# Kernel tuning notes

Hardware: AMD Instinct MI355X
Metric: run time of the kernel (lower is better)

## Reference

```python
import jax, jax.numpy as jnp
import numpy as np

BAND = 8          # band_width
DS = 0.1          # diag_subtract
DILATIONS = (1, 2, 4)
EPS_NORM = 1e-6
EPS_GAP = 1e-6
EPS_LN = 1e-5


def _conv1d(x, w, b, dil=1):
    # x: (B, C_in, T), w: (C_out, C_in, K) torch-style OIH
    pad = dil * (w.shape[-1] // 2)  # 'same' padding as in torch module
    y = jax.lax.conv_general_dilated(
        x, w, window_strides=(1,), padding=[(pad, pad)],
        rhs_dilation=(dil,), dimension_numbers=("NCH", "OIH", "NCH"))
    return y + b[None, :, None]


def _strip(feat, mask, w, ds):
    # Banded cosine SSM: strip[b, idx, t] = ((xn[b,t].xn[b,t+|k|]) - ds*[k==0] + 1)/2 * m[t]*m[t+|k|]
    # Mathematically identical to full S = xn xn^T (symmetric) followed by
    # extract_diagonal_strip, but computes only the (2w+1)-wide band.
    xm = feat * mask[:, :, None]
    xn = xm / (jnp.linalg.norm(xm, axis=-1, keepdims=True) + EPS_NORM)
    T = xn.shape[1]
    rows = []
    for k in range(-w, w + 1):
        a = abs(k)
        dot = jnp.einsum("btd,btd->bt", xn[:, :T - a] if a else xn, xn[:, a:])
        s = (dot - (ds if k == 0 else 0.0) + 1.0) * 0.5
        s = s * mask[:, :T - a] * mask[:, a:] if a else s * mask * mask
        rows.append(jnp.pad(s, ((0, 0), (0, a))))
    return jnp.stack(rows, axis=1)  # (B, 2w+1, T)


def _encode(strip, mask, w_in, b_in, stages):
    h = jax.nn.relu(_conv1d(strip, w_in, b_in))
    for (wd, bd, wp, bp, d) in stages:
        h = jax.nn.relu(_conv1d(h, wd, bd, d))   # dilated k=3 conv (dropout=eval no-op)
        h = jax.nn.relu(_conv1d(h, wp, bp))      # pointwise k=1 conv
    m = mask[:, None, :]
    return (h * m).sum(-1) / (m.sum(-1) + EPS_GAP)  # masked GAP -> (B, C)


def setup_inputs() -> dict:
    key = jax.random.key(0)
    ks = jax.random.split(key, 32)
    B, T, D, C, NB = 32, 4096, 256, 64, 2 * BAND + 1
    s = 0.02
    n = lambda k, shp: (jax.random.normal(k, shp, jnp.float32) * s)
    inp = {
        "video_feat": jax.random.normal(ks[0], (B, T, D), jnp.float32),
        "audio_feat": jax.random.normal(ks[1], (B, T, D), jnp.float32),
        "video_mask": jnp.ones((B, T), jnp.float32),
        "audio_mask": jnp.ones((B, T), jnp.float32),
        "w_in": n(ks[2], (C, NB, 1)), "b_in": jnp.zeros((C,), jnp.float32),
        "w_d1": n(ks[3], (C, C, 3)), "b_d1": jnp.zeros((C,), jnp.float32),
        "w_p1": n(ks[4], (C, C, 1)), "b_p1": jnp.zeros((C,), jnp.float32),
        "w_d2": n(ks[5], (C, C, 3)), "b_d2": jnp.zeros((C,), jnp.float32),
        "w_p2": n(ks[6], (C, C, 1)), "b_p2": jnp.zeros((C,), jnp.float32),
        "w_d3": n(ks[7], (C, C, 3)), "b_d3": jnp.zeros((C,), jnp.float32),
        "w_p3": n(ks[8], (C, C, 1)), "b_p3": jnp.zeros((C,), jnp.float32),
        "ln_g": jnp.ones((2 * C,), jnp.float32), "ln_b": jnp.zeros((2 * C,), jnp.float32),
        "mha_w1": n(ks[9], (2 * C, C)), "mha_b1": jnp.zeros((C,), jnp.float32),
        "mha_w2": n(ks[10], (C, 1)), "mha_b2": -jnp.ones((1,), jnp.float32),
        "ffn_w1": n(ks[11], (2 * C, C)), "ffn_b1": jnp.zeros((C,), jnp.float32),
        "ffn_w2": n(ks[12], (C, 1)), "ffn_b2": jnp.zeros((1,), jnp.float32),
    }
    return inp


def reference(video_feat, audio_feat, video_mask, audio_mask,
              w_in, b_in, w_d1, b_d1, w_p1, b_p1, w_d2, b_d2, w_p2, b_p2,
              w_d3, b_d3, w_p3, b_p3, ln_g, ln_b,
              mha_w1, mha_b1, mha_w2, mha_b2, ffn_w1, ffn_b1, ffn_w2, ffn_b2):
    stages = [(w_d1, b_d1, w_p1, b_p1, DILATIONS[0]),
              (w_d2, b_d2, w_p2, b_p2, DILATIONS[1]),
              (w_d3, b_d3, w_p3, b_p3, DILATIONS[2])]
    z_a = _encode(_strip(audio_feat, audio_mask, BAND, DS), audio_mask, w_in, b_in, stages)
    z_v = _encode(_strip(video_feat, video_mask, BAND, DS), video_mask, w_in, b_in, stages)
    f = jnp.concatenate([z_a, z_v], axis=-1)  # (B, 2C), audio first as in torch
    mu = f.mean(-1, keepdims=True)
    var = ((f - mu) ** 2).mean(-1, keepdims=True)
    fn = (f - mu) / jnp.sqrt(var + EPS_LN) * ln_g + ln_b
    g_mha = jax.nn.sigmoid(jax.nn.relu(fn @ mha_w1 + mha_b1) @ mha_w2 + mha_b2)
    g_ffn = jnp.tanh(jax.nn.relu(fn @ ffn_w1 + ffn_b1) @ ffn_w2 + ffn_b2)
    return (g_mha[:, :, None], g_ffn[:, :, None])  # (B,1,1) each
```

## Files before the change

kernel.cpp:

```cpp
#include <hip/hip_runtime.h>
#include <math.h>

#define B_ 32
#define T_ 4096
#define D_ 256
#define C_ 64
#define EPSN 1e-6f
#define EPSG 1e-6f
#define EPSL 1e-5f
#define DS_ 0.1f

typedef short bfrag __attribute__((ext_vector_type(8)));
typedef float f32x4 __attribute__((ext_vector_type(4)));
typedef unsigned short ushort4_t __attribute__((ext_vector_type(4)));
typedef unsigned short ushort8_t __attribute__((ext_vector_type(8)));

static __device__ __forceinline__ unsigned short f2bf(float f) {
    unsigned int u = __builtin_bit_cast(unsigned int, f);
    unsigned int r = u + 0x7fffu + ((u >> 16) & 1u);
    return (unsigned short)(r >> 16);
}
static __device__ __forceinline__ float bf2f(unsigned short u) {
    return __builtin_bit_cast(float, ((unsigned int)u) << 16);
}

static __device__ __forceinline__ f32x4 mfma_bf16(bfrag a, bfrag b, f32x4 c) {
    return __builtin_amdgcn_mfma_f32_16x16x32_bf16(a, b, c, 0, 0, 0);
}

static __device__ __forceinline__ bfrag cvt8(float4 lo, float4 hi) {
    bfrag v;
    v[0] = (short)f2bf(lo.x); v[1] = (short)f2bf(lo.y);
    v[2] = (short)f2bf(lo.z); v[3] = (short)f2bf(lo.w);
    v[4] = (short)f2bf(hi.x); v[5] = (short)f2bf(hi.y);
    v[6] = (short)f2bf(hi.z); v[7] = (short)f2bf(hi.w);
    return v;
}

static __device__ __forceinline__ unsigned int cvtpk(float a, float b) {
    unsigned int r;
    asm("v_cvt_pk_bf16_f32 %0, %1, %2" : "=v"(r) : "v"(a), "v"(b));
    return r;
}

#define GLD16(dst, base, OFF) \
    asm volatile("global_load_dwordx4 %0, %1, off offset:" #OFF \
                 : "=v"(dst) : "v"(base))

__global__ __launch_bounds__(256) void prepack_kernel(
    const float* __restrict__ w_in,
    const float* __restrict__ wd0, const float* __restrict__ wp0,
    const float* __restrict__ wd1, const float* __restrict__ wp1,
    const float* __restrict__ wd2, const float* __restrict__ wp2,
    unsigned short* __restrict__ wk)
{
    int idx = blockIdx.x * 256 + threadIdx.x;
    if (idx >= 1024 + 3 * 16384) return;
    if (idx < 1024) {
        int c = idx >> 4, a = idx & 15;
        float wv = 0.f;
        if (a <= 8) {
            wv = w_in[c * 17 + 8 + a];
            if (a > 0) wv += w_in[c * 17 + 8 - a];
        }
        wk[idx] = f2bf(wv);
    } else {
        int i2 = idx - 1024;
        int s = i2 >> 14;
        int r = i2 & 16383;
        const float* wd = s == 0 ? wd0 : (s == 1 ? wd1 : wd2);
        const float* wp = s == 0 ? wp0 : (s == 1 ? wp1 : wp2);
        unsigned short v;
        if (r < 12288) {
            int c = r / 192, k = r - c * 192;
            int tap = k >> 6, ci = k & 63;
            v = f2bf(wd[c * 192 + ci * 3 + tap]);
        } else {
            v = f2bf(wp[r - 12288]);
        }
        wk[idx] = v;
    }
}

#define SEQB 22
#define TPB 2

__global__ __launch_bounds__(256, 2) void strip_kernel(
    const float* __restrict__ feat0, const float* __restrict__ mask0,
    const float* __restrict__ feat1, const float* __restrict__ mask1,
    unsigned short* __restrict__ s16g)
{
    __shared__ float dotbuf[4 * 864];
    __shared__ float sclw[4 * 32];
    __shared__ float mskb[208];

    int bid0 = blockIdx.x;
    int bid  = (bid0 & 7) * 176 + (bid0 >> 3);
    int seq  = bid / SEQB;
    int blk  = bid - seq * SEQB;
    int b    = seq & 31;
    int mod  = seq >> 5;
    int mb   = mod * B_ + b;
    const float* feat = mod ? feat1 : feat0;
    const float* mask = mod ? mask1 : mask0;
    int first = blk * TPB;
    int ngr   = (43 - first < TPB) ? (43 - first) : TPB;
    int base0 = first * 96;
    int tid = threadIdx.x;
    int w = tid >> 6, lane = tid & 63;
    int l15 = lane & 15, lg = lane >> 4;

    if (tid < 208) {
        int tg = base0 + tid;
        mskb[tid] = (tg < T_) ? mask[(size_t)b * T_ + tg] : 0.f;
    }
    __syncthreads();

    const float* fb = feat + (size_t)b * T_ * D_;

    float4 fa0[8], fb0[8], fa1[8], fb1[8];
    const float *pA, *pB;

    auto setaddr = [&](int g) {
        int i0 = (first + g) * 96 + 24 * w;
        int tA = i0 + l15;      if (tA >= T_) tA = 0;
        int tB = i0 + 16 + l15; if (tB >= T_) tB = 0;
        pA = fb + (size_t)tA * D_ + lg * 8;
        pB = fb + (size_t)tB * D_ + lg * 8;
    };

#define ISSUE_C0() do { \
    GLD16(fa0[0], pA, 0);   GLD16(fb0[0], pB, 0);   \
    GLD16(fa0[1], pA, 16);  GLD16(fb0[1], pB, 16);  \
    GLD16(fa0[2], pA, 128); GLD16(fb0[2], pB, 128); \
    GLD16(fa0[3], pA, 144); GLD16(fb0[3], pB, 144); \
    GLD16(fa0[4], pA, 256); GLD16(fb0[4], pB, 256); \
    GLD16(fa0[5], pA, 272); GLD16(fb0[5], pB, 272); \
    GLD16(fa0[6], pA, 384); GLD16(fb0[6], pB, 384); \
    GLD16(fa0[7], pA, 400); GLD16(fb0[7], pB, 400); } while (0)

#define ISSUE_C1() do { \
    GLD16(fa1[0], pA, 512); GLD16(fb1[0], pB, 512); \
    GLD16(fa1[1], pA, 528); GLD16(fb1[1], pB, 528); \
    GLD16(fa1[2], pA, 640); GLD16(fb1[2], pB, 640); \
    GLD16(fa1[3], pA, 656); GLD16(fb1[3], pB, 656); \
    GLD16(fa1[4], pA, 768); GLD16(fb1[4], pB, 768); \
    GLD16(fa1[5], pA, 784); GLD16(fb1[5], pB, 784); \
    GLD16(fa1[6], pA, 896); GLD16(fb1[6], pB, 896); \
    GLD16(fa1[7], pA, 912); GLD16(fb1[7], pB, 912); } while (0)

    setaddr(0);
    ISSUE_C0();
    ISSUE_C1();

    for (int g = 0; g < ngr; ++g) {
        bool nxt = (g + 1 < ngr);

        __builtin_amdgcn_sched_barrier(0);
        asm volatile("s_waitcnt vmcnt(16)" ::: "memory");
        __builtin_amdgcn_sched_barrier(0);

        f32x4 a00 = {0.f, 0.f, 0.f, 0.f};
        f32x4 a01 = {0.f, 0.f, 0.f, 0.f};
        f32x4 a11 = {0.f, 0.f, 0.f, 0.f};
        #pragma unroll
        for (int ks = 0; ks < 4; ++ks) {
            bfrag av = cvt8(fa0[2 * ks], fa0[2 * ks + 1]);
            bfrag bv = cvt8(fb0[2 * ks], fb0[2 * ks + 1]);
            a00 = mfma_bf16(av, av, a00);
            a01 = mfma_bf16(av, bv, a01);
            a11 = mfma_bf16(bv, bv, a11);
        }

        if (nxt) { setaddr(g + 1); ISSUE_C0(); }

        __builtin_amdgcn_sched_barrier(0);
        if (nxt) asm volatile("s_waitcnt vmcnt(16)" ::: "memory");
        else     asm volatile("s_waitcnt vmcnt(0)"  ::: "memory");
        __builtin_amdgcn_sched_barrier(0);

        #pragma unroll
        for (int ks = 0; ks < 4; ++ks) {
            bfrag av = cvt8(fa1[2 * ks], fa1[2 * ks + 1]);
            bfrag bv = cvt8(fb1[2 * ks], fb1[2 * ks + 1]);
            a00 = mfma_bf16(av, av, a00);
            a01 = mfma_bf16(av, bv, a01);
            a11 = mfma_bf16(bv, bv, a11);
        }

        if (nxt) ISSUE_C1();

        int i0 = (first + g) * 96 + 24 * w;
        float* bb = dotbuf + w * 864;
        #pragma unroll
        for (int r = 0; r < 4; ++r) {
            int row = lg * 4 + r;
            bb[row * 18 + l15] = a00[r];
            bb[288 + row * 18 + l15] = a01[r];
            bb[576 + row * 18 + l15] = a11[r];
        }
        if (lane < 32) {
            int v = lane;
            float sd = (v < 16) ? bb[v * 18 + v] : bb[576 + (v - 16) * 18 + (v - 16)];
            float m = mskb[i0 - base0 + v];
            sclw[w * 32 + v] = m / (m * sqrtf(sd) + EPSN);
        }
        if (lane < 24) {
            int r = lane;
            int tglob = i0 + r;
            if (tglob < T_) {
                int rel = i0 - base0 + r;
                float m_t = mskb[rel], sc_t = sclw[w * 32 + r];
                ushort8_t o0, o1;
                #pragma unroll
                for (int e = 0; e < 8; ++e) { o0[e] = 0; o1[e] = 0; }
                #pragma unroll
                for (int a = 0; a <= 8; ++a) {
                    int c = r + a;
                    float dot;
                    if (r < 8)       dot = bb[r * 18 + c];
                    else if (r < 16) dot = (c < 16) ? bb[r * 18 + c]
                                                   : bb[288 + r * 18 + (c - 16)];
                    else             dot = bb[576 + (r - 16) * 18 + (c - 16)];
                    float dn = dot * sc_t * sclw[w * 32 + r + a];
                    float s = (dn - (a == 0 ? DS_ : 0.f) + 1.f) * 0.5f * m_t * mskb[rel + a];
                    if (a < 8) o0[a] = f2bf(s); else o1[0] = f2bf(s);
                }
                unsigned short* dst = s16g + ((size_t)mb * T_ + tglob) * 16;
                *(ushort8_t*)dst = o0;
                *(ushort8_t*)(dst + 8) = o1;
            }
        }
    }
#undef ISSUE_C0
#undef ISSUE_C1
}

#define TT 128
#define G_ 16
#define WB 160
#define OFF_BUFA 1024
#define OFF_BUFB 21504
#define SMEM_TOT (41984 + 512)

static __device__ __forceinline__ int swzi(int row, int su, int off) {
    return row * 64 + ((su ^ (row & 7)) << 3) + off;
}

static __device__ __forceinline__ void emit4(unsigned short* dst, f32x4 acc, bool valid) {
    float v0 = valid ? fmaxf(acc[0], 0.f) : 0.f;
    float v1 = valid ? fmaxf(acc[1], 0.f) : 0.f;
    float v2 = valid ? fmaxf(acc[2], 0.f) : 0.f;
    float v3 = valid ? fmaxf(acc[3], 0.f) : 0.f;
    uint2 p;
    p.x = cvtpk(v0, v1);
    p.y = cvtpk(v2, v3);
    *(uint2*)dst = p;
}

template<int DIL>
static __device__ __forceinline__ void conv_stage(
    const unsigned short* __restrict__ wdg, const unsigned short* __restrict__ wpg,
    unsigned short* __restrict__ bufIn, unsigned short* __restrict__ bufOut,
    const float* __restrict__ b_d, const float* __restrict__ b_p,
    int t0, int l15, int lg, int mt0, int wn)
{
    {
        bfrag ad[2][6];
        f32x4 bd[2];
        #pragma unroll
        for (int m = 0; m < 2; ++m) {
            int row = (mt0 + m) * 16 + l15;
            #pragma unroll
            for (int ks = 0; ks < 6; ++ks) {
                int tap = ks >> 1, half = ks & 1;
                ad[m][ks] = *(const bfrag*)(wdg + row * 192 + tap * 64 + half * 32 + lg * 8);
            }
            #pragma unroll
            for (int r = 0; r < 4; ++r) bd[m][r] = b_d[(mt0 + m) * 16 + lg * 4 + r];
        }
        for (int nt = wn * 5; nt < wn * 5 + 5; ++nt) {
            int j = nt * 16 + l15;
            f32x4 acc0 = bd[0], acc1 = bd[1];
            #pragma unroll
            for (int ks = 0; ks < 6; ++ks) {
                int tap = ks >> 1, half = ks & 1;
                int brow = j + (tap - 1) * DIL;
                bfrag bv = *(const bfrag*)(bufIn + swzi(brow, half * 4 + lg, 0));
                acc0 = mfma_bf16(ad[0][ks], bv, acc0);
                acc1 = mfma_bf16(ad[1][ks], bv, acc1);
            }
            int tg = t0 - G_ + j;
            bool valid = (tg >= 0 && tg < T_);
            emit4(bufOut + swzi(j, (mt0 + 0) * 2 + (lg >> 1), (lg & 1) * 4), acc0, valid);
            emit4(bufOut + swzi(j, (mt0 + 1) * 2 + (lg >> 1), (lg & 1) * 4), acc1, valid);
        }
    }
    __syncthreads();

    {
        bfrag ap[2][2];
        f32x4 bp[2];
        #pragma unroll
        for (int m = 0; m < 2; ++m) {
            int row = (mt0 + m) * 16 + l15;
            #pragma unroll
            for (int half = 0; half < 2; ++half)
                ap[m][half] = *(const bfrag*)(wpg + row * 64 + half * 32 + lg * 8);
            #pragma unroll
            for (int r = 0; r < 4; ++r) bp[m][r] = b_p[(mt0 + m) * 16 + lg * 4 + r];
        }
        for (int nt = wn * 5; nt < wn * 5 + 5; ++nt) {
            int j = nt * 16 + l15;
            f32x4 acc0 = bp[0], acc1 = bp[1];
            #pragma unroll
            for (int half = 0; half < 2; ++half) {
                bfrag bv = *(const bfrag*)(bufOut + swzi(j, half * 4 + lg, 0));
                acc0 = mfma_bf16(ap[0][half], bv, acc0);
                acc1 = mfma_bf16(ap[1][half], bv, acc1);
            }
            int tg = t0 - G_ + j;
            bool valid = (tg >= 0 && tg < T_);
            emit4(bufIn + swzi(j, (mt0 + 0) * 2 + (lg >> 1), (lg & 1) * 4), acc0, valid);
            emit4(bufIn + swzi(j, (mt0 + 1) * 2 + (lg >> 1), (lg & 1) * 4), acc1, valid);
        }
    }
    __syncthreads();
}

__global__ __launch_bounds__(256, 3) void conv_mfma_kernel(
    const unsigned short* __restrict__ s16g,
    const float* __restrict__ mask0, const float* __restrict__ mask1,
    const unsigned short* __restrict__ wk,
    const float* __restrict__ b_in,
    const float* __restrict__ b_d1, const float* __restrict__ b_p1,
    const float* __restrict__ b_d2, const float* __restrict__ b_p2,
    const float* __restrict__ b_d3, const float* __restrict__ b_p3,
    float* __restrict__ z_part)
{
    __shared__ __align__(16) char smem[SMEM_TOT];
    float* red = (float*)smem;
    unsigned short* bufA = (unsigned short*)(smem + OFF_BUFA);
    unsigned short* bufB = (unsigned short*)(smem + OFF_BUFB);

    int bid  = blockIdx.x;
    int tile = bid & 31;
    int b    = (bid >> 5) & 31;
    int mod  = bid >> 10;
    int mb   = mod * B_ + b;
    const float* mask = mod ? mask1 : mask0;
    int t0  = tile * TT;
    int tid = threadIdx.x;
    int lane = tid & 63;
    int w = tid >> 6;
    int l15 = lane & 15, lg = lane >> 4;
    int wm = w >> 1, wn = w & 1;
    int mt0 = wm * 2;

    {
        const unsigned short* srow = s16g + (size_t)mb * T_ * 16;
        int lg2 = lg & 1;
        bfrag a_in[2];
        f32x4 bi[2];
        #pragma unroll
        for (int m = 0; m < 2; ++m) {
            int row = (mt0 + m) * 16 + l15;
            a_in[m] = *(const bfrag*)(wk + row * 16 + lg2 * 8);
            #pragma unroll
            for (int r = 0; r < 4; ++r) bi[m][r] = b_in[(mt0 + m) * 16 + lg * 4 + r];
        }
        for (int nt = wn * 5; nt < wn * 5 + 5; ++nt) {
            int j = nt * 16 + l15;
            int tg = t0 - G_ + j;
            bool valid = (tg >= 0 && tg < T_);
            bfrag bv = {0, 0, 0, 0, 0, 0, 0, 0};
            if (lg < 2 && valid) bv = *(const bfrag*)(srow + (size_t)tg * 16 + lg * 8);
            f32x4 acc0 = bi[0], acc1 = bi[1];
            acc0 = mfma_bf16(a_in[0], bv, acc0);
            acc1 = mfma_bf16(a_in[1], bv, acc1);
            emit4(bufA + swzi(j, (mt0 + 0) * 2 + (lg >> 1), (lg & 1) * 4), acc0, valid);
            emit4(bufA + swzi(j, (mt0 + 1) * 2 + (lg >> 1), (lg & 1) * 4), acc1, valid);
        }
    }
    __syncthreads();

    conv_stage<1>(wk + 1024,             wk + 1024 + 12288,             bufA, bufB, b_d1, b_p1, t0, l15, lg, mt0, wn);
    conv_stage<2>(wk + 1024 + 16384,     wk + 1024 + 16384 + 12288,     bufA, bufB, b_d2, b_p2, t0, l15, lg, mt0, wn);
    conv_stage<4>(wk + 1024 + 2 * 16384, wk + 1024 + 2 * 16384 + 12288, bufA, bufB, b_d3, b_p3, t0, l15, lg, mt0, wn);

    {
        int c = tid & 63, g = tid >> 6;
        const float* mrow = mask + (size_t)b * T_ + t0;
        float acc = 0.f;
        #pragma unroll 4
        for (int i = 0; i < 32; ++i) {
            int jj = g * 32 + i;
            int r = G_ + jj;
            acc += bf2f(bufA[swzi(r, c >> 3, c & 7)]) * mrow[jj];
        }
        red[g * 64 + c] = acc;
    }
    __syncthreads();
    if (tid < 64) {
        float z = red[tid] + red[64 + tid] + red[128 + tid] + red[192 + tid];
        z_part[((size_t)mb * 32 + tile) * 64 + tid] = z;
    }
}

__global__ __launch_bounds__(128) void gates_kernel(
    const float* __restrict__ z_part,
    const float* __restrict__ mask0, const float* __restrict__ mask1,
    const float* __restrict__ ln_g, const float* __restrict__ ln_b,
    const float* __restrict__ mha_w1, const float* __restrict__ mha_b1,
    const float* __restrict__ mha_w2, const float* __restrict__ mha_b2,
    const float* __restrict__ ffn_w1, const float* __restrict__ ffn_b1,
    const float* __restrict__ ffn_w2, const float* __restrict__ ffn_b2,
    float* __restrict__ out)
{
    __shared__ float fn[128];
    __shared__ float red[4];
    __shared__ float msum[2];
    int b = blockIdx.x, tid = threadIdx.x;
    int mod = tid >> 6, c = tid & 63;

    float z = 0.f;
    for (int tl = 0; tl < 32; ++tl)
        z += z_part[((size_t)(mod * B_ + b) * 32 + tl) * 64 + c];

    const float* mk = mod ? mask1 : mask0;
    float ms = 0.f;
    for (int t = c; t < T_; t += 64) ms += mk[(size_t)b * T_ + t];
    #pragma unroll
    for (int o = 32; o > 0; o >>= 1) ms += __shfl_xor(ms, o);
    if (c == 0) msum[mod] = ms;
    __syncthreads();

    float fv = z / (msum[mod] + EPSG);
    float s1 = fv, s2 = fv * fv;
    #pragma unroll
    for (int o = 32; o > 0; o >>= 1) { s1 += __shfl_xor(s1, o); s2 += __shfl_xor(s2, o); }
    if (c == 0) { red[mod * 2] = s1; red[mod * 2 + 1] = s2; }
    __syncthreads();

    float mu  = (red[0] + red[2]) * (1.0f / 128.0f);
    float ex2 = (red[1] + red[3]) * (1.0f / 128.0f);
    float var = ex2 - mu * mu;
    float fnv = (fv - mu) * rsqrtf(var + EPSL) * ln_g[tid] + ln_b[tid];
    fn[tid] = fnv;
    __syncthreads();

    const float* W1 = mod ? ffn_w1 : mha_w1;
    const float* B1 = mod ? ffn_b1 : mha_b1;
    const float* W2 = mod ? ffn_w2 : mha_w2;
    const float* B2 = mod ? ffn_b2 : mha_b2;
    float r = B1[c];
    for (int i = 0; i < 128; ++i) r += fn[i] * W1[i * 64 + c];
    r = fmaxf(r, 0.f);
    float g = r * W2[c];
    #pragma unroll
    for (int o = 32; o > 0; o >>= 1) g += __shfl_xor(g, o);
    if (c == 0) {
        g += B2[0];
        out[mod * B_ + b] = mod ? tanhf(g) : 1.0f / (1.0f + expf(-g));
    }
}

extern "C" void kernel_launch(void* const* d_in, const int* in_sizes, int n_in,
                              void* d_out, int out_size, void* d_ws, size_t ws_size,
                              hipStream_t stream) {
    const float* video_feat = (const float*)d_in[0];
    const float* audio_feat = (const float*)d_in[1];
    const float* video_mask = (const float*)d_in[2];
    const float* audio_mask = (const float*)d_in[3];
    const float* w_in = (const float*)d_in[4];
    const float* b_in = (const float*)d_in[5];
    const float* w_d1 = (const float*)d_in[6];
    const float* b_d1 = (const float*)d_in[7];
    const float* w_p1 = (const float*)d_in[8];
    const float* b_p1 = (const float*)d_in[9];
    const float* w_d2 = (const float*)d_in[10];
    const float* b_d2 = (const float*)d_in[11];
    const float* w_p2 = (const float*)d_in[12];
    const float* b_p2 = (const float*)d_in[13];
    const float* w_d3 = (const float*)d_in[14];
    const float* b_d3 = (const float*)d_in[15];
    const float* w_p3 = (const float*)d_in[16];
    const float* b_p3 = (const float*)d_in[17];
    const float* ln_g = (const float*)d_in[18];
    const float* ln_b = (const float*)d_in[19];
    const float* mha_w1 = (const float*)d_in[20];
    const float* mha_b1 = (const float*)d_in[21];
    const float* mha_w2 = (const float*)d_in[22];
    const float* mha_b2 = (const float*)d_in[23];
    const float* ffn_w1 = (const float*)d_in[24];
    const float* ffn_b1 = (const float*)d_in[25];
    const float* ffn_w2 = (const float*)d_in[26];
    const float* ffn_b2 = (const float*)d_in[27];

    unsigned short* s16g = (unsigned short*)d_ws;
    float* z_part = (float*)((char*)d_ws + (size_t)2 * B_ * T_ * 16 * 2);
    unsigned short* wk = (unsigned short*)((char*)z_part + (size_t)2 * B_ * 32 * 64 * 4);

    prepack_kernel<<<dim3(196), dim3(256), 0, stream>>>(
        w_in, w_d1, w_p1, w_d2, w_p2, w_d3, w_p3, wk);

    strip_kernel<<<dim3(64 * SEQB), dim3(256), 0, stream>>>(
        audio_feat, audio_mask, video_feat, video_mask, s16g);

    conv_mfma_kernel<<<dim3(2 * B_ * (T_ / TT)), dim3(256), 0, stream>>>(
        s16g, audio_mask, video_mask, wk, b_in,
        b_d1, b_p1, b_d2, b_p2, b_d3, b_p3, z_part);

    gates_kernel<<<dim3(B_), dim3(128), 0, stream>>>(
        z_part, audio_mask, video_mask, ln_g, ln_b,
        mha_w1, mha_b1, mha_w2, mha_b2, ffn_w1, ffn_b1, ffn_w2, ffn_b2,
        (float*)d_out);
}
```

Baseline: 144.7 us.

## Fuse banded cosine strip computation into conv encoder kernel via LDS

Merges the strip kernel into the conv encoder kernel so each 128-step tile computes its own strip rows (with a 16-step halo) directly into shared memory instead of writing a bf16 strip tensor to global memory and reading it back. This removes one kernel launch and the global round trip of the strip intermediate. In exchange, halo rows are recomputed per tile (176 rows for 128 outputs), so feature reads and MFMA dot work grow, and shared memory use per block rises.

After: 189.0 us. 1.31x slower.

```diff
diff --git a/kernel.cpp b/kernel.cpp
--- a/kernel.cpp
+++ b/kernel.cpp
@@ -82,52 +82,155 @@
     }
 }
 
-#define SEQB 22
-#define TPB 2
-
-__global__ __launch_bounds__(256, 2) void strip_kernel(
+#define TT 128
+#define G_ 16
+#define OFF_BUFA 1024
+#define OFF_BUFB 21504
+#define OFF_SBUF 41984
+#define OFF_MSKB 47360
+#define SMEM_TOT 48576
+
+static __device__ __forceinline__ int swzi(int row, int su, int off) {
+    return row * 64 + ((su ^ (row & 7)) << 3) + off;
+}
+
+static __device__ __forceinline__ void emit4(unsigned short* dst, f32x4 acc, bool valid) {
+    float v0 = valid ? fmaxf(acc[0], 0.f) : 0.f;
+    float v1 = valid ? fmaxf(acc[1], 0.f) : 0.f;
+    float v2 = valid ? fmaxf(acc[2], 0.f) : 0.f;
+    float v3 = valid ? fmaxf(acc[3], 0.f) : 0.f;
+    uint2 p;
+    p.x = cvtpk(v0, v1);
+    p.y = cvtpk(v2, v3);
+    *(uint2*)dst = p;
+}
+
+template<int DIL>
+static __device__ __forceinline__ void conv_stage(
+    const unsigned short* __restrict__ wdg, const unsigned short* __restrict__ wpg,
+    unsigned short* __restrict__ bufIn, unsigned short* __restrict__ bufOut,
+    const float* __restrict__ b_d, const float* __restrict__ b_p,
+    int t0, int l15, int lg, int mt0, int wn)
+{
+    {
+        bfrag ad[2][6];
+        f32x4 bd[2];
+        #pragma unroll
+        for (int m = 0; m < 2; ++m) {
+            int row = (mt0 + m) * 16 + l15;
+            #pragma unroll
+            for (int ks = 0; ks < 6; ++ks) {
+                int tap = ks >> 1, half = ks & 1;
+                ad[m][ks] = *(const bfrag*)(wdg + row * 192 + tap * 64 + half * 32 + lg * 8);
+            }
+            #pragma unroll
+            for (int r = 0; r < 4; ++r) bd[m][r] = b_d[(mt0 + m) * 16 + lg * 4 + r];
+        }
+        for (int nt = wn * 5; nt < wn * 5 + 5; ++nt) {
+            int j = nt * 16 + l15;
+            f32x4 acc0 = bd[0], acc1 = bd[1];
+            #pragma unroll
+            for (int ks = 0; ks < 6; ++ks) {
+                int tap = ks >> 1, half = ks & 1;
+                int brow = j + (tap - 1) * DIL;
+                bfrag bv = *(const bfrag*)(bufIn + swzi(brow, half * 4 + lg, 0));
+                acc0 = mfma_bf16(ad[0][ks], bv, acc0);
+                acc1 = mfma_bf16(ad[1][ks], bv, acc1);
+            }
+            int tg = t0 - G_ + j;
+            bool valid = (tg >= 0 && tg < T_);
+            emit4(bufOut + swzi(j, (mt0 + 0) * 2 + (lg >> 1), (lg & 1) * 4), acc0, valid);
+            emit4(bufOut + swzi(j, (mt0 + 1) * 2 + (lg >> 1), (lg & 1) * 4), acc1, valid);
+        }
+    }
+    __syncthreads();
+
+    {
+        bfrag ap[2][2];
+        f32x4 bp[2];
+        #pragma unroll
+        for (int m = 0; m < 2; ++m) {
+            int row = (mt0 + m) * 16 + l15;
+            #pragma unroll
+            for (int half = 0; half < 2; ++half)
+                ap[m][half] = *(const bfrag*)(wpg + row * 64 + half * 32 + lg * 8);
+            #pragma unroll
+            for (int r = 0; r < 4; ++r) bp[m][r] = b_p[(mt0 + m) * 16 + lg * 4 + r];
+        }
+        for (int nt = wn * 5; nt < wn * 5 + 5; ++nt) {
+            int j = nt * 16 + l15;
+            f32x4 acc0 = bp[0], acc1 = bp[1];
+            #pragma unroll
+            for (int half = 0; half < 2; ++half) {
+                bfrag bv = *(const bfrag*)(bufOut + swzi(j, half * 4 + lg, 0));
+                acc0 = mfma_bf16(ap[0][half], bv, acc0);
+                acc1 = mfma_bf16(ap[1][half], bv, acc1);
+            }
+            int tg = t0 - G_ + j;
+            bool valid = (tg >= 0 && tg < T_);
+            emit4(bufIn + swzi(j, (mt0 + 0) * 2 + (lg >> 1), (lg & 1) * 4), acc0, valid);
+            emit4(bufIn + swzi(j, (mt0 + 1) * 2 + (lg >> 1), (lg & 1) * 4), acc1, valid);
+        }
+    }
+    __syncthreads();
+}
+
+__global__ __launch_bounds__(256, 3) void fused_kernel(
     const float* __restrict__ feat0, const float* __restrict__ mask0,
     const float* __restrict__ feat1, const float* __restrict__ mask1,
-    unsigned short* __restrict__ s16g)
+    const unsigned short* __restrict__ wk,
+    const float* __restrict__ b_in,
+    const float* __restrict__ b_d1, const float* __restrict__ b_p1,
+    const float* __restrict__ b_d2, const float* __restrict__ b_p2,
+    const float* __restrict__ b_d3, const float* __restrict__ b_p3,
+    float* __restrict__ z_part)
 {
-    __shared__ float dotbuf[4 * 864];
-    __shared__ float sclw[4 * 32];
-    __shared__ float mskb[208];
+    __shared__ __align__(16) char smem[SMEM_TOT];
+    float* red = (float*)smem;
+    unsigned short* bufA = (unsigned short*)(smem + OFF_BUFA);
+    unsigned short* bufB = (unsigned short*)(smem + OFF_BUFB);
+    float* dotbuf = (float*)(smem + OFF_BUFB);
+    float* sclw   = dotbuf + 4 * 864;
+    unsigned short* sbuf = (unsigned short*)(smem + OFF_SBUF);
+    float* mskb = (float*)(smem + OFF_MSKB);
 
     int bid0 = blockIdx.x;
-    int bid  = (bid0 & 7) * 176 + (bid0 >> 3);
-    int seq  = bid / SEQB;
-    int blk  = bid - seq * SEQB;
-    int b    = seq & 31;
-    int mod  = seq >> 5;
+    int bid  = (bid0 & 7) * 256 + (bid0 >> 3);
+    int tile = bid & 31;
+    int b    = (bid >> 5) & 31;
+    int mod  = bid >> 10;
     int mb   = mod * B_ + b;
     const float* feat = mod ? feat1 : feat0;
     const float* mask = mod ? mask1 : mask0;
-    int first = blk * TPB;
-    int ngr   = (43 - first < TPB) ? (43 - first) : TPB;
-    int base0 = first * 96;
+    int t0  = tile * TT;
+    int g0  = t0 - G_;
     int tid = threadIdx.x;
-    int w = tid >> 6, lane = tid & 63;
+    int lane = tid & 63;
+    int w = tid >> 6;
     int l15 = lane & 15, lg = lane >> 4;
-
-    if (tid < 208) {
-        int tg = base0 + tid;
-        mskb[tid] = (tg < T_) ? mask[(size_t)b * T_ + tg] : 0.f;
-    }
-    __syncthreads();
-
-    const float* fb = feat + (size_t)b * T_ * D_;
-
-    float4 fa0[8], fb0[8], fa1[8], fb1[8];
-    const float *pA, *pB;
-
-    auto setaddr = [&](int g) {
-        int i0 = (first + g) * 96 + 24 * w;
-        int tA = i0 + l15;      if (tA >= T_) tA = 0;
-        int tB = i0 + 16 + l15; if (tB >= T_) tB = 0;
-        pA = fb + (size_t)tA * D_ + lg * 8;
-        pB = fb + (size_t)tB * D_ + lg * 8;
-    };
+    int wm = w >> 1, wn = w & 1;
+    int mt0 = wm * 2;
+
+    if (tid < 176) {
+        int tg = g0 + tid;
+        mskb[tid] = (tg >= 0 && tg < T_) ? mask[(size_t)b * T_ + tg] : 0.f;
+    }
+    __syncthreads();
+
+    {
+        const float* fbp = feat + (size_t)b * T_ * D_;
+        int ngr = (w < 3) ? 2 : 1;
+
+        float4 fa0[8], fb0[8], fa1[8], fb1[8];
+        const float *pA, *pB;
+
+        auto setaddr = [&](int g) {
+            int i0l = 24 * g;
+            int tA = g0 + i0l + l15;      if (tA < 0 || tA >= T_) tA = 0;
+            int tB = g0 + i0l + 16 + l15; if (tB < 0 || tB >= T_) tB = 0;
+            pA = fbp + (size_t)tA * D_ + lg * 8;
+            pB = fbp + (size_t)tB * D_ + lg * 8;
+        };
 
 #define ISSUE_C0() do { \
     GLD16(fa0[0], pA, 0);   GLD16(fb0[0], pB, 0);   \
@@ -149,67 +252,66 @@
     GLD16(fa1[6], pA, 896); GLD16(fb1[6], pB, 896); \
     GLD16(fa1[7], pA, 912); GLD16(fb1[7], pB, 912); } while (0)
 
-    setaddr(0);
-    ISSUE_C0();
-    ISSUE_C1();
-
-    for (int g = 0; g < ngr; ++g) {
-        bool nxt = (g + 1 < ngr);
-
-        __builtin_amdgcn_sched_barrier(0);
-        asm volatile("s_waitcnt vmcnt(16)" ::: "memory");
-        __builtin_amdgcn_sched_barrier(0);
-
-        f32x4 a00 = {0.f, 0.f, 0.f, 0.f};
-        f32x4 a01 = {0.f, 0.f, 0.f, 0.f};
-        f32x4 a11 = {0.f, 0.f, 0.f, 0.f};
-        #pragma unroll
-        for (int ks = 0; ks < 4; ++ks) {
-            bfrag av = cvt8(fa0[2 * ks], fa0[2 * ks + 1]);
-            bfrag bv = cvt8(fb0[2 * ks], fb0[2 * ks + 1]);
-            a00 = mfma_bf16(av, av, a00);
-            a01 = mfma_bf16(av, bv, a01);
-            a11 = mfma_bf16(bv, bv, a11);
-        }
-
-        if (nxt) { setaddr(g + 1); ISSUE_C0(); }
-
-        __builtin_amdgcn_sched_barrier(0);
-        if (nxt) asm volatile("s_waitcnt vmcnt(16)" ::: "memory");
-        else     asm volatile("s_waitcnt vmcnt(0)"  ::: "memory");
-        __builtin_amdgcn_sched_barrier(0);
-
-        #pragma unroll
-        for (int ks = 0; ks < 4; ++ks) {
-            bfrag av = cvt8(fa1[2 * ks], fa1[2 * ks + 1]);
-            bfrag bv = cvt8(fb1[2 * ks], fb1[2 * ks + 1]);
-            a00 = mfma_bf16(av, av, a00);
-            a01 = mfma_bf16(av, bv, a01);
-            a11 = mfma_bf16(bv, bv, a11);
-        }
-
-        if (nxt) ISSUE_C1();
-
-        int i0 = (first + g) * 96 + 24 * w;
-        float* bb = dotbuf + w * 864;
-        #pragma unroll
-        for (int r = 0; r < 4; ++r) {
-            int row = lg * 4 + r;
-            bb[row * 18 + l15] = a00[r];
-            bb[288 + row * 18 + l15] = a01[r];
-            bb[576 + row * 18 + l15] = a11[r];
-        }
-        if (lane < 32) {
-            int v = lane;
-            float sd = (v < 16) ? bb[v * 18 + v] : bb[576 + (v - 16) * 18 + (v - 16)];
-            float m = mskb[i0 - base0 + v];
-            sclw[w * 32 + v] = m / (m * sqrtf(sd) + EPSN);
-        }
-        if (lane < 24) {
-            int r = lane;
-            int tglob = i0 + r;
-            if (tglob < T_) {
-                int rel = i0 - base0 + r;
+        setaddr(w);
+        ISSUE_C0();
+        ISSUE_C1();
+
+        for (int k = 0; k < ngr; ++k) {
+            int g = (k == 0) ? w : w + 4;
+            bool nxt = (k + 1 < ngr);
+
+            __builtin_amdgcn_sched_barrier(0);
+            asm volatile("s_waitcnt vmcnt(16)" ::: "memory");
+            __builtin_amdgcn_sched_barrier(0);
+
+            f32x4 a00 = {0.f, 0.f, 0.f, 0.f};
+            f32x4 a01 = {0.f, 0.f, 0.f, 0.f};
+            f32x4 a11 = {0.f, 0.f, 0.f, 0.f};
+            #pragma unroll
+            for (int ks = 0; ks < 4; ++ks) {
+                bfrag av = cvt8(fa0[2 * ks], fa0[2 * ks + 1]);
+                bfrag bv = cvt8(fb0[2 * ks], fb0[2 * ks + 1]);
+                a00 = mfma_bf16(av, av, a00);
+                a01 = mfma_bf16(av, bv, a01);
+                a11 = mfma_bf16(bv, bv, a11);
+            }
+
+            if (nxt) { setaddr(w + 4); ISSUE_C0(); }
+
+            __builtin_amdgcn_sched_barrier(0);
+            if (nxt) asm volatile("s_waitcnt vmcnt(16)" ::: "memory");
+            else     asm volatile("s_waitcnt vmcnt(0)"  ::: "memory");
+            __builtin_amdgcn_sched_barrier(0);
+
+            #pragma unroll
+            for (int ks = 0; ks < 4; ++ks) {
+                bfrag av = cvt8(fa1[2 * ks], fa1[2 * ks + 1]);
+                bfrag bv = cvt8(fb1[2 * ks], fb1[2 * ks + 1]);
+                a00 = mfma_bf16(av, av, a00);
+                a01 = mfma_bf16(av, bv, a01);
+                a11 = mfma_bf16(bv, bv, a11);
+            }
+
+            if (nxt) ISSUE_C1();
+
+            int i0l = 24 * g;
+            float* bb = dotbuf + w * 864;
+            #pragma unroll
+            for (int r = 0; r < 4; ++r) {
+                int row = lg * 4 + r;
+                bb[row * 18 + l15] = a00[r];
+                bb[288 + row * 18 + l15] = a01[r];
+                bb[576 + row * 18 + l15] = a11[r];
+            }
+            if (lane < 32) {
+                int v = lane;
+                float sd = (v < 16) ? bb[v * 18 + v] : bb[576 + (v - 16) * 18 + (v - 16)];
+                float m = mskb[i0l + v];
+                sclw[w * 32 + v] = m / (m * sqrtf(sd) + EPSN);
+            }
+            if (lane < 24) {
+                int r = lane;
+                int rel = i0l + r;
                 float m_t = mskb[rel], sc_t = sclw[w * 32 + r];
                 ushort8_t o0, o1;
                 #pragma unroll
@@ -226,139 +328,17 @@
                     float s = (dn - (a == 0 ? DS_ : 0.f) + 1.f) * 0.5f * m_t * mskb[rel + a];
                     if (a < 8) o0[a] = f2bf(s); else o1[0] = f2bf(s);
                 }
-                unsigned short* dst = s16g + ((size_t)mb * T_ + tglob) * 16;
+                unsigned short* dst = sbuf + rel * 16;
                 *(ushort8_t*)dst = o0;
                 *(ushort8_t*)(dst + 8) = o1;
             }
         }
-    }
 #undef ISSUE_C0
 #undef ISSUE_C1
-}
-
-#define TT 128
-#define G_ 16
-#define WB 160
-#define OFF_BUFA 1024
-#define OFF_BUFB 21504
-#define SMEM_TOT (41984 + 512)
-
-static __device__ __forceinline__ int swzi(int row, int su, int off) {
-    return row * 64 + ((su ^ (row & 7)) << 3) + off;
-}
-
-static __device__ __forceinline__ void emit4(unsigned short* dst, f32x4 acc, bool valid) {
-    float v0 = valid ? fmaxf(acc[0], 0.f) : 0.f;
-    float v1 = valid ? fmaxf(acc[1], 0.f) : 0.f;
-    float v2 = valid ? fmaxf(acc[2], 0.f) : 0.f;
-    float v3 = valid ? fmaxf(acc[3], 0.f) : 0.f;
-    uint2 p;
-    p.x = cvtpk(v0, v1);
-    p.y = cvtpk(v2, v3);
-    *(uint2*)dst = p;
-}
-
-template<int DIL>
-static __device__ __forceinline__ void conv_stage(
-    const unsigned short* __restrict__ wdg, const unsigned short* __restrict__ wpg,
-    unsigned short* __restrict__ bufIn, unsigned short* __restrict__ bufOut,
-    const float* __restrict__ b_d, const float* __restrict__ b_p,
-    int t0, int l15, int lg, int mt0, int wn)
-{
+    }
+    __syncthreads();
+
     {
-        bfrag ad[2][6];
-        f32x4 bd[2];
-        #pragma unroll
-        for (int m = 0; m < 2; ++m) {
-            int row = (mt0 + m) * 16 + l15;
-            #pragma unroll
-            for (int ks = 0; ks < 6; ++ks) {
-                int tap = ks >> 1, half = ks & 1;
-                ad[m][ks] = *(const bfrag*)(wdg + row * 192 + tap * 64 + half * 32 + lg * 8);
-            }
-            #pragma unroll
-            for (int r = 0; r < 4; ++r) bd[m][r] = b_d[(mt0 + m) * 16 + lg * 4 + r];
-        }
-        for (int nt = wn * 5; nt < wn * 5 + 5; ++nt) {
-            int j = nt * 16 + l15;
-            f32x4 acc0 = bd[0], acc1 = bd[1];
-            #pragma unroll
-            for (int ks = 0; ks < 6; ++ks) {
-                int tap = ks >> 1, half = ks & 1;
-                int brow = j + (tap - 1) * DIL;
-                bfrag bv = *(const bfrag*)(bufIn + swzi(brow, half * 4 + lg, 0));
-                acc0 = mfma_bf16(ad[0][ks], bv, acc0);
-                acc1 = mfma_bf16(ad[1][ks], bv, acc1);
-            }
-            int tg = t0 - G_ + j;
-            bool valid = (tg >= 0 && tg < T_);
-            emit4(bufOut + swzi(j, (mt0 + 0) * 2 + (lg >> 1), (lg & 1) * 4), acc0, valid);
-            emit4(bufOut + swzi(j, (mt0 + 1) * 2 + (lg >> 1), (lg & 1) * 4), acc1, valid);
-        }
-    }
-    __syncthreads();
-
-    {
-        bfrag ap[2][2];
-        f32x4 bp[2];
-        #pragma unroll
-        for (int m = 0; m < 2; ++m) {
-            int row = (mt0 + m) * 16 + l15;
-            #pragma unroll
-            for (int half = 0; half < 2; ++half)
-                ap[m][half] = *(const bfrag*)(wpg + row * 64 + half * 32 + lg * 8);
-            #pragma unroll
-            for (int r = 0; r < 4; ++r) bp[m][r] = b_p[(mt0 + m) * 16 + lg * 4 + r];
-        }
-        for (int nt = wn * 5; nt < wn * 5 + 5; ++nt) {
-            int j = nt * 16 + l15;
-            f32x4 acc0 = bp[0], acc1 = bp[1];
-            #pragma unroll
-            for (int half = 0; half < 2; ++half) {
-                bfrag bv = *(const bfrag*)(bufOut + swzi(j, half * 4 + lg, 0));
-                acc0 = mfma_bf16(ap[0][half], bv, acc0);
-                acc1 = mfma_bf16(ap[1][half], bv, acc1);
-            }
-            int tg = t0 - G_ + j;
-            bool valid = (tg >= 0 && tg < T_);
-            emit4(bufIn + swzi(j, (mt0 + 0) * 2 + (lg >> 1), (lg & 1) * 4), acc0, valid);
-            emit4(bufIn + swzi(j, (mt0 + 1) * 2 + (lg >> 1), (lg & 1) * 4), acc1, valid);
-        }
-    }
-    __syncthreads();
-}
-
-__global__ __launch_bounds__(256, 3) void conv_mfma_kernel(
-    const unsigned short* __restrict__ s16g,
-    const float* __restrict__ mask0, const float* __restrict__ mask1,
-    const unsigned short* __restrict__ wk,
-    const float* __restrict__ b_in,
-    const float* __restrict__ b_d1, const float* __restrict__ b_p1,
-    const float* __restrict__ b_d2, const float* __restrict__ b_p2,
-    const float* __restrict__ b_d3, const float* __restrict__ b_p3,
-    float* __restrict__ z_part)
-{
-    __shared__ __align__(16) char smem[SMEM_TOT];
-    float* red = (float*)smem;
-    unsigned short* bufA = (unsigned short*)(smem + OFF_BUFA);
-    unsigned short* bufB = (unsigned short*)(smem + OFF_BUFB);
-
-    int bid  = blockIdx.x;
-    int tile = bid & 31;
-    int b    = (bid >> 5) & 31;
-    int mod  = bid >> 10;
-    int mb   = mod * B_ + b;
-    const float* mask = mod ? mask1 : mask0;
-    int t0  = tile * TT;
-    int tid = threadIdx.x;
-    int lane = tid & 63;
-    int w = tid >> 6;
-    int l15 = lane & 15, lg = lane >> 4;
-    int wm = w >> 1, wn = w & 1;
-    int mt0 = wm * 2;
-
-    {
-        const unsigned short* srow = s16g + (size_t)mb * T_ * 16;
         int lg2 = lg & 1;
         bfrag a_in[2];
         f32x4 bi[2];
@@ -374,7 +354,7 @@
             int tg = t0 - G_ + j;
             bool valid = (tg >= 0 && tg < T_);
             bfrag bv = {0, 0, 0, 0, 0, 0, 0, 0};
-            if (lg < 2 && valid) bv = *(const bfrag*)(srow + (size_t)tg * 16 + lg * 8);
+            if (lg < 2) bv = *(const bfrag*)(sbuf + j * 16 + lg * 8);
             f32x4 acc0 = bi[0], acc1 = bi[1];
             acc0 = mfma_bf16(a_in[0], bv, acc0);
             acc1 = mfma_bf16(a_in[1], bv, acc1);
@@ -497,18 +477,14 @@
     const float* ffn_w2 = (const float*)d_in[26];
     const float* ffn_b2 = (const float*)d_in[27];
 
-    unsigned short* s16g = (unsigned short*)d_ws;
-    float* z_part = (float*)((char*)d_ws + (size_t)2 * B_ * T_ * 16 * 2);
-    unsigned short* wk = (unsigned short*)((char*)z_part + (size_t)2 * B_ * 32 * 64 * 4);
+    float* z_part = (float*)d_ws;
+    unsigned short* wk = (unsigned short*)((char*)d_ws + (size_t)2 * B_ * 32 * 64 * 4);
 
     prepack_kernel<<<dim3(196), dim3(256), 0, stream>>>(
         w_in, w_d1, w_p1, w_d2, w_p2, w_d3, w_p3, wk);
 
-    strip_kernel<<<dim3(64 * SEQB), dim3(256), 0, stream>>>(
-        audio_feat, audio_mask, video_feat, video_mask, s16g);
-
-    conv_mfma_kernel<<<dim3(2 * B_ * (T_ / TT)), dim3(256), 0, stream>>>(
-        s16g, audio_mask, video_mask, wk, b_in,
+    fused_kernel<<<dim3(2 * B_ * (T_ / TT)), dim3(256), 0, stream>>>(
+        audio_feat, audio_mask, video_feat, video_mask, wk, b_in,
         b_d1, b_p1, b_d2, b_p2, b_d3, b_p3, z_part);
 
     gates_kernel<<<dim3(B_), dim3(128), 0, stream>>>(
```
